# Kernel tuning notes

Measured on AMD Instinct MI355X. Metric: run time of the kernel, lower is better.

The kernel has to match this reference:

```python
import jax, jax.numpy as jnp
import numpy as np

ALPHA = 0.3
B, T, I, H = 256, 1024, 128, 1024


def setup_inputs() -> dict:
    key = jax.random.key(0)
    ks = jax.random.split(key, 7)
    s = 1.0 / np.sqrt(H)
    return {
        "x": jax.random.normal(ks[0], (B, T, I), dtype=jnp.float32),
        "W_ih": jax.random.normal(ks[1], (3 * H, I), dtype=jnp.float32) * s,
        "W_hh": jax.random.normal(ks[2], (3 * H, H), dtype=jnp.float32) * s,
        "b_ih": jax.random.normal(ks[3], (3 * H,), dtype=jnp.float32) * s,
        "b_hh": jax.random.normal(ks[4], (3 * H,), dtype=jnp.float32) * s,
        "W_fc": jax.random.normal(ks[5], (2, H), dtype=jnp.float32) * s,
        "b_fc": jax.random.normal(ks[6], (2,), dtype=jnp.float32) * s,
    }


def _forward(x, W_ih, W_hh, b_ih, b_hh, W_fc, b_fc):
    # --- ES normalize: s_i = (1-a)*x_i + a*s_{i-1}, s_0 = x_0 (in-place EMA) ---
    xs = jnp.swapaxes(x, 0, 1)  # [T, B, I]
    s0 = xs[0]

    def ema_step(s, xi):
        s2 = (1.0 - ALPHA) * xi + ALPHA * s
        return s2, s2

    _, rest = jax.lax.scan(ema_step, s0, xs[1:])
    sm = jnp.concatenate([s0[None], rest], axis=0)  # [T, B, I] smoothed
    st_1 = sm[-1]  # [B, I]

    # --- GRU (single layer, batch_first, h0 = 0); gate order r, z, n ---
    gi = jnp.einsum('tbi,gi->tbg', sm, W_ih) + b_ih  # [T, B, 3H]
    h0 = jnp.zeros((x.shape[0], W_hh.shape[1]), dtype=x.dtype)

    def gru_step(h, gi_t):
        gh = h @ W_hh.T + b_hh  # [B, 3H]
        i_r, i_z, i_n = jnp.split(gi_t, 3, axis=-1)
        h_r, h_z, h_n = jnp.split(gh, 3, axis=-1)
        r = jax.nn.sigmoid(i_r + h_r)
        z = jax.nn.sigmoid(i_z + h_z)
        n = jnp.tanh(i_n + r * h_n)
        h2 = (1.0 - z) * n + z * h
        return h2, None

    h_out, _ = jax.lax.scan(gru_step, h0, gi)  # [B, H]

    out = h_out @ W_fc.T + b_fc  # [B, 2]
    # --- ES denormalize with columns [1, 2] of st_1 ---
    out = (out - ALPHA * st_1[:, 1:3]) / (1.0 - ALPHA)
    return out


def reference(x, W_ih, W_hh, b_ih, b_hh, W_fc, b_fc):
    return _forward(x, W_ih, W_hh, b_ih, b_hh, W_fc, b_fc)
```

## Files before the change

kernel.cpp:

```cpp
#include <hip/hip_runtime.h>

typedef __attribute__((ext_vector_type(4))) float f4;
typedef __attribute__((ext_vector_type(8))) short frag8;
typedef unsigned long long u64;
typedef unsigned int u32;
typedef unsigned short u16;

#define ALPHA 0.3f

#define WHH_OFF   0ull
#define WIH_OFF   6291456ull
#define HBUF_OFF  7077888ull
#define CTR_OFF   8126464ull
#define ST1_OFF   8159232ull
#define ZERO_LEN  1083392ull

__device__ __forceinline__ u16 f2bf(float f) {
  u32 u = __float_as_uint(f);
  u32 r = (u + 0x7FFFu + ((u >> 16) & 1u)) >> 16;
  return (u16)r;
}
__device__ __forceinline__ float bf2f(u16 h) {
  return __uint_as_float(((u32)h) << 16);
}
__device__ __forceinline__ float sigmf(float x) {
  float e = __expf(-fabsf(x));
  float s = 1.0f / (1.0f + e);
  return x >= 0.f ? s : 1.0f - s;
}
__device__ __forceinline__ float tanhf_(float x) {
  float e = __expf(-2.0f * fabsf(x));
  float t = (1.0f - e) / (1.0f + e);
  return x >= 0.f ? t : -t;
}
__device__ __forceinline__ frag8 pack_bf16(f4 a, f4 b) {
  union { u16 h[8]; frag8 f; } u;
  u.h[0] = f2bf(a[0]); u.h[1] = f2bf(a[1]); u.h[2] = f2bf(a[2]); u.h[3] = f2bf(a[3]);
  u.h[4] = f2bf(b[0]); u.h[5] = f2bf(b[1]); u.h[6] = f2bf(b[2]); u.h[7] = f2bf(b[3]);
  return u.f;
}

__global__ void prep_bf16(const float* __restrict__ whh_f32,
                          const float* __restrict__ wih_f32,
                          u16* __restrict__ whh, u16* __restrict__ wih) {
  int i = blockIdx.x * 256 + threadIdx.x;
  const int nhh = 3072 * 1024;
  if (i < nhh) whh[i] = f2bf(whh_f32[i]);
  else         wih[i - nhh] = f2bf(wih_f32[i - nhh]);
}

__global__ __launch_bounds__(256, 1) void gru_kernel(
    const float* __restrict__ x,
    const float* __restrict__ b_ih,
    const float* __restrict__ b_hh,
    const u16* __restrict__ whh,
    const u16* __restrict__ wih,
    u64* __restrict__ hbuf,
    u32* __restrict__ ctr,
    float* __restrict__ st1)
{
  __shared__ f4 xbuf[4096];
  const int wg = blockIdx.x;
  const int g = wg >> 5, w = wg & 31;
  const int tid = threadIdx.x;
  const int v = tid >> 6;
  const int l = tid & 63;
  const int lm = l & 15, lq = l >> 4;

  frag8 whhf[8][6];
  frag8 wihf[6];
#pragma unroll
  for (int rt = 0; rt < 6; ++rt) {
    int grow = (rt >> 1) * 1024 + w * 32 + (rt & 1) * 16 + lm;
    wihf[rt] = *(const frag8*)(wih + grow * 128 + v * 32 + lq * 8);
#pragma unroll
    for (int kb = 0; kb < 8; ++kb)
      whhf[kb][rt] = *(const frag8*)(whh + grow * 1024 + v * 256 + kb * 32 + lq * 8);
  }

  const int uc = tid & 31;
  const int ub0 = (tid >> 5) << 2;
  const int colg = w * 32 + uc;
  const float bir = b_ih[colg],         bhr = b_hh[colg];
  const float biz = b_ih[1024 + colg],  bhz = b_hh[1024 + colg];
  const float bin_ = b_ih[2048 + colg], bhn = b_hh[2048 + colg];
  f4 hprev = {0.f, 0.f, 0.f, 0.f};

  f4 e0a, e0b, e1a, e1b;
  const float* xb0 = x + (size_t)(g * 32 + lm) * 131072 + v * 32 + lq * 8;
  const float* xb1 = x + (size_t)(g * 32 + 16 + lm) * 131072 + v * 32 + lq * 8;

  u32* cbase = ctr + g * 1024;
  const f4 zz = {0.f, 0.f, 0.f, 0.f};
  const float A1 = 1.0f - ALPHA;

#pragma unroll 1
  for (int t = 0; t < 1024; ++t) {
    u64* hread  = hbuf + (size_t)((t & 1) * 8 + g) * 8192;
    u64* hwrite = hbuf + (size_t)(((t + 1) & 1) * 8 + g) * 8192;

    frag8 af[8][2];
#pragma unroll
    for (int kb = 0; kb < 8; ++kb) {
#pragma unroll
      for (int bh = 0; bh < 2; ++bh) {
        int base = (((8 * v + kb) * 2 + bh) * 64 + l) * 2;
        union { u64 q[2]; frag8 f; } uu;
        uu.q[0] = __hip_atomic_load(hread + base,     __ATOMIC_RELAXED, __HIP_MEMORY_SCOPE_AGENT);
        uu.q[1] = __hip_atomic_load(hread + base + 1, __ATOMIC_RELAXED, __HIP_MEMORY_SCOPE_AGENT);
        af[kb][bh] = uu.f;
      }
    }

    {
      const float* xp0 = xb0 + (size_t)t * 128;
      const float* xp1 = xb1 + (size_t)t * 128;
      f4 xa0 = *(const f4*)xp0, xc0 = *(const f4*)(xp0 + 4);
      f4 xa1 = *(const f4*)xp1, xc1 = *(const f4*)(xp1 + 4);
      if (t == 0) { e0a = xa0; e0b = xc0; e1a = xa1; e1b = xc1; }
      else {
        e0a = A1 * xa0 + ALPHA * e0a; e0b = A1 * xc0 + ALPHA * e0b;
        e1a = A1 * xa1 + ALPHA * e1a; e1b = A1 * xc1 + ALPHA * e1b;
      }
    }
    if (t == 1023 && w == 0 && v == 0 && lq == 0) {
      st1[(g * 32 + lm) * 2 + 0] = e0a[1];
      st1[(g * 32 + lm) * 2 + 1] = e0a[2];
      st1[(g * 32 + 16 + lm) * 2 + 0] = e1a[1];
      st1[(g * 32 + 16 + lm) * 2 + 1] = e1a[2];
    }
    frag8 smf0 = pack_bf16(e0a, e0b);
    frag8 smf1 = pack_bf16(e1a, e1b);

    f4 acc[2][6], accn[2][2];
#pragma unroll
    for (int bh = 0; bh < 2; ++bh) {
#pragma unroll
      for (int rt = 0; rt < 6; ++rt) acc[bh][rt] = zz;
      accn[bh][0] = zz; accn[bh][1] = zz;
    }
#pragma unroll
    for (int rt = 0; rt < 4; ++rt) {
      acc[0][rt] = __builtin_amdgcn_mfma_f32_16x16x32_bf16(smf0, wihf[rt], acc[0][rt], 0, 0, 0);
      acc[1][rt] = __builtin_amdgcn_mfma_f32_16x16x32_bf16(smf1, wihf[rt], acc[1][rt], 0, 0, 0);
    }
#pragma unroll
    for (int nt = 0; nt < 2; ++nt) {
      accn[0][nt] = __builtin_amdgcn_mfma_f32_16x16x32_bf16(smf0, wihf[4 + nt], accn[0][nt], 0, 0, 0);
      accn[1][nt] = __builtin_amdgcn_mfma_f32_16x16x32_bf16(smf1, wihf[4 + nt], accn[1][nt], 0, 0, 0);
    }
#pragma unroll
    for (int kb = 0; kb < 8; ++kb) {
#pragma unroll
      for (int rt = 0; rt < 6; ++rt) {
        acc[0][rt] = __builtin_amdgcn_mfma_f32_16x16x32_bf16(af[kb][0], whhf[kb][rt], acc[0][rt], 0, 0, 0);
        acc[1][rt] = __builtin_amdgcn_mfma_f32_16x16x32_bf16(af[kb][1], whhf[kb][rt], acc[1][rt], 0, 0, 0);
      }
    }

#pragma unroll
    for (int bh = 0; bh < 2; ++bh) {
      int b8 = bh * 4 + lq;
#pragma unroll
      for (int rt = 0; rt < 6; ++rt) {
        int gr = rt * 16 + lm;
        xbuf[((v * 128 + gr) << 3) | (b8 ^ (gr & 7))] = acc[bh][rt];
      }
#pragma unroll
      for (int nt = 0; nt < 2; ++nt) {
        int gr = 96 + nt * 16 + lm;
        xbuf[((v * 128 + gr) << 3) | (b8 ^ (gr & 7))] = accn[bh][nt];
      }
    }
    __syncthreads();

    int swz = (ub0 >> 2) ^ (uc & 7);
    f4 sr = zz, sz4 = zz, gn4 = zz, gin4 = zz;
#pragma unroll
    for (int vv = 0; vv < 4; ++vv) {
      sr   += xbuf[((vv * 128 + uc) << 3) | swz];
      sz4  += xbuf[((vv * 128 + 32 + uc) << 3) | swz];
      gn4  += xbuf[((vv * 128 + 64 + uc) << 3) | swz];
      gin4 += xbuf[((vv * 128 + 96 + uc) << 3) | swz];
    }
    f4 h4;
#pragma unroll
    for (int i = 0; i < 4; ++i) {
      float rr = sigmf(sr[i] + bir + bhr);
      float zg = sigmf(sz4[i] + biz + bhz);
      float nn = tanhf_(gin4[i] + bin_ + rr * (gn4[i] + bhn));
      h4[i] = (1.0f - zg) * nn + zg * hprev[i];
    }
    hprev = h4;
    __syncthreads();

    u16* sbuf = (u16*)&xbuf[0];
#pragma unroll
    for (int i = 0; i < 4; ++i) sbuf[(ub0 + i) * 40 + uc] = f2bf(h4[i]);
    __syncthreads();
    {
      int b = tid >> 3, c0 = (tid & 7) << 2;
      u64 pk = *(const u64*)(sbuf + b * 40 + c0);
      int off = ((w * 2 + (b >> 4)) * 64 + (b & 15) + 16 * (c0 >> 3)) * 2 + ((c0 & 7) >> 2);
      __hip_atomic_store(hwrite + off, pk, __ATOMIC_RELAXED, __HIP_MEMORY_SCOPE_AGENT);
    }
    __syncthreads();

    if (tid == 0) {
      u32* cp = cbase + t;
      __hip_atomic_fetch_add(cp, 1u, __ATOMIC_RELEASE, __HIP_MEMORY_SCOPE_AGENT);
      while (__hip_atomic_load(cp, __ATOMIC_RELAXED, __HIP_MEMORY_SCOPE_AGENT) < 32u)
        __builtin_amdgcn_s_sleep(2);
      __builtin_amdgcn_fence(__ATOMIC_ACQUIRE, "agent");
    }
    __syncthreads();
  }
}

__global__ void fc_kernel(const u16* __restrict__ hbuf_bf,
                          const float* __restrict__ wfc,
                          const float* __restrict__ bfc,
                          const float* __restrict__ st1,
                          float* __restrict__ out)
{
  int b = blockIdx.x, t = threadIdx.x;
  int g = b >> 5, bl = b & 31, bh = bl >> 4;
  int k0 = t * 4, kb = k0 >> 5, ko = k0 & 31;
  int lane = (bl & 15) + 16 * (ko >> 3);
  const u16* hp = hbuf_bf + (size_t)g * 32768 + ((kb * 2 + bh) * 64 + lane) * 8 + (ko & 7);
  float h0 = bf2f(hp[0]), h1 = bf2f(hp[1]), h2 = bf2f(hp[2]), h3 = bf2f(hp[3]);
  float s0 = h0 * wfc[k0] + h1 * wfc[k0 + 1] + h2 * wfc[k0 + 2] + h3 * wfc[k0 + 3];
  float s1 = h0 * wfc[1024 + k0] + h1 * wfc[1024 + k0 + 1] +
             h2 * wfc[1024 + k0 + 2] + h3 * wfc[1024 + k0 + 3];
#pragma unroll
  for (int off = 32; off > 0; off >>= 1) {
    s0 += __shfl_down(s0, off);
    s1 += __shfl_down(s1, off);
  }
  __shared__ float red[8];
  if ((t & 63) == 0) { red[(t >> 6) * 2] = s0; red[(t >> 6) * 2 + 1] = s1; }
  __syncthreads();
  if (t == 0) {
    float a0 = red[0] + red[2] + red[4] + red[6] + bfc[0];
    float a1 = red[1] + red[3] + red[5] + red[7] + bfc[1];
    float inv = 1.0f / (1.0f - ALPHA);
    out[b * 2 + 0] = (a0 - ALPHA * st1[b * 2 + 0]) * inv;
    out[b * 2 + 1] = (a1 - ALPHA * st1[b * 2 + 1]) * inv;
  }
}

extern "C" void kernel_launch(void* const* d_in, const int* in_sizes, int n_in,
                              void* d_out, int out_size, void* d_ws, size_t ws_size,
                              hipStream_t stream) {
  const float* x   = (const float*)d_in[0];
  const float* Wih = (const float*)d_in[1];
  const float* Whh = (const float*)d_in[2];
  const float* bih = (const float*)d_in[3];
  const float* bhh = (const float*)d_in[4];
  const float* Wfc = (const float*)d_in[5];
  const float* bfc = (const float*)d_in[6];
  char* ws = (char*)d_ws;
  u16* whh_bf = (u16*)(ws + WHH_OFF);
  u16* wih_bf = (u16*)(ws + WIH_OFF);
  u64* hbuf   = (u64*)(ws + HBUF_OFF);
  u32* ctr    = (u32*)(ws + CTR_OFF);
  float* st1  = (float*)(ws + ST1_OFF);

  hipMemsetAsync(ws + HBUF_OFF, 0, ZERO_LEN, stream);
  prep_bf16<<<13824, 256, 0, stream>>>(Whh, Wih, whh_bf, wih_bf);
  gru_kernel<<<256, 256, 0, stream>>>(x, bih, bhh, whh_bf, wih_bf, hbuf, ctr, st1);
  fc_kernel<<<256, 256, 0, stream>>>((const u16*)(ws + HBUF_OFF), Wfc, bfc, st1,
                                     (float*)d_out);
}
```

Measured before the change: 9.300 ms.

## Replace atomic counter barrier with per-workgroup flags and overlap input projection

Measured after the change: 11.53 ms. +24.0%, slower.

```diff
diff --git a/kernel.cpp b/kernel.cpp
--- a/kernel.cpp
+++ b/kernel.cpp
@@ -11,9 +11,9 @@
 #define WHH_OFF   0ull
 #define WIH_OFF   6291456ull
 #define HBUF_OFF  7077888ull
-#define CTR_OFF   8126464ull
-#define ST1_OFF   8159232ull
-#define ZERO_LEN  1083392ull
+#define FLG_OFF   8126464ull
+#define ST1_OFF   8128512ull
+#define ZERO_LEN  1052672ull
 
 __device__ __forceinline__ u16 f2bf(float f) {
   u32 u = __float_as_uint(f);
@@ -56,10 +56,11 @@
     const u16* __restrict__ whh,
     const u16* __restrict__ wih,
     u64* __restrict__ hbuf,
-    u32* __restrict__ ctr,
+    u32* __restrict__ flags,
     float* __restrict__ st1)
 {
   __shared__ f4 xbuf[4096];
+  __shared__ u16 sbuf[32 * 40];
   const int wg = blockIdx.x;
   const int g = wg >> 5, w = wg & 31;
   const int tid = threadIdx.x;
@@ -90,9 +91,43 @@
   const float* xb0 = x + (size_t)(g * 32 + lm) * 131072 + v * 32 + lq * 8;
   const float* xb1 = x + (size_t)(g * 32 + 16 + lm) * 131072 + v * 32 + lq * 8;
 
-  u32* cbase = ctr + g * 1024;
+  u32* fbase = flags + g * 64;
   const f4 zz = {0.f, 0.f, 0.f, 0.f};
   const float A1 = 1.0f - ALPHA;
+
+  f4 acc[2][6], accn[2][2];
+
+  auto gi_compute = [&](int tt) {
+    const float* xp0 = xb0 + (size_t)tt * 128;
+    const float* xp1 = xb1 + (size_t)tt * 128;
+    f4 xa0 = *(const f4*)xp0, xc0 = *(const f4*)(xp0 + 4);
+    f4 xa1 = *(const f4*)xp1, xc1 = *(const f4*)(xp1 + 4);
+    if (tt == 0) { e0a = xa0; e0b = xc0; e1a = xa1; e1b = xc1; }
+    else {
+      e0a = A1 * xa0 + ALPHA * e0a; e0b = A1 * xc0 + ALPHA * e0b;
+      e1a = A1 * xa1 + ALPHA * e1a; e1b = A1 * xc1 + ALPHA * e1b;
+    }
+    frag8 smf0 = pack_bf16(e0a, e0b);
+    frag8 smf1 = pack_bf16(e1a, e1b);
+#pragma unroll
+    for (int bh = 0; bh < 2; ++bh) {
+#pragma unroll
+      for (int rt = 0; rt < 6; ++rt) acc[bh][rt] = zz;
+      accn[bh][0] = zz; accn[bh][1] = zz;
+    }
+#pragma unroll
+    for (int rt = 0; rt < 4; ++rt) {
+      acc[0][rt] = __builtin_amdgcn_mfma_f32_16x16x32_bf16(smf0, wihf[rt], acc[0][rt], 0, 0, 0);
+      acc[1][rt] = __builtin_amdgcn_mfma_f32_16x16x32_bf16(smf1, wihf[rt], acc[1][rt], 0, 0, 0);
+    }
+#pragma unroll
+    for (int nt = 0; nt < 2; ++nt) {
+      accn[0][nt] = __builtin_amdgcn_mfma_f32_16x16x32_bf16(smf0, wihf[4 + nt], accn[0][nt], 0, 0, 0);
+      accn[1][nt] = __builtin_amdgcn_mfma_f32_16x16x32_bf16(smf1, wihf[4 + nt], accn[1][nt], 0, 0, 0);
+    }
+  };
+
+  gi_compute(0);
 
 #pragma unroll 1
   for (int t = 0; t < 1024; ++t) {
@@ -111,44 +146,6 @@
         af[kb][bh] = uu.f;
       }
     }
-
-    {
-      const float* xp0 = xb0 + (size_t)t * 128;
-      const float* xp1 = xb1 + (size_t)t * 128;
-      f4 xa0 = *(const f4*)xp0, xc0 = *(const f4*)(xp0 + 4);
-      f4 xa1 = *(const f4*)xp1, xc1 = *(const f4*)(xp1 + 4);
-      if (t == 0) { e0a = xa0; e0b = xc0; e1a = xa1; e1b = xc1; }
-      else {
-        e0a = A1 * xa0 + ALPHA * e0a; e0b = A1 * xc0 + ALPHA * e0b;
-        e1a = A1 * xa1 + ALPHA * e1a; e1b = A1 * xc1 + ALPHA * e1b;
-      }
-    }
-    if (t == 1023 && w == 0 && v == 0 && lq == 0) {
-      st1[(g * 32 + lm) * 2 + 0] = e0a[1];
-      st1[(g * 32 + lm) * 2 + 1] = e0a[2];
-      st1[(g * 32 + 16 + lm) * 2 + 0] = e1a[1];
-      st1[(g * 32 + 16 + lm) * 2 + 1] = e1a[2];
-    }
-    frag8 smf0 = pack_bf16(e0a, e0b);
-    frag8 smf1 = pack_bf16(e1a, e1b);
-
-    f4 acc[2][6], accn[2][2];
-#pragma unroll
-    for (int bh = 0; bh < 2; ++bh) {
-#pragma unroll
-      for (int rt = 0; rt < 6; ++rt) acc[bh][rt] = zz;
-      accn[bh][0] = zz; accn[bh][1] = zz;
-    }
-#pragma unroll
-    for (int rt = 0; rt < 4; ++rt) {
-      acc[0][rt] = __builtin_amdgcn_mfma_f32_16x16x32_bf16(smf0, wihf[rt], acc[0][rt], 0, 0, 0);
-      acc[1][rt] = __builtin_amdgcn_mfma_f32_16x16x32_bf16(smf1, wihf[rt], acc[1][rt], 0, 0, 0);
-    }
-#pragma unroll
-    for (int nt = 0; nt < 2; ++nt) {
-      accn[0][nt] = __builtin_amdgcn_mfma_f32_16x16x32_bf16(smf0, wihf[4 + nt], accn[0][nt], 0, 0, 0);
-      accn[1][nt] = __builtin_amdgcn_mfma_f32_16x16x32_bf16(smf1, wihf[4 + nt], accn[1][nt], 0, 0, 0);
-    }
 #pragma unroll
     for (int kb = 0; kb < 8; ++kb) {
 #pragma unroll
@@ -192,9 +189,7 @@
       h4[i] = (1.0f - zg) * nn + zg * hprev[i];
     }
     hprev = h4;
-    __syncthreads();
-
-    u16* sbuf = (u16*)&xbuf[0];
+
 #pragma unroll
     for (int i = 0; i < 4; ++i) sbuf[(ub0 + i) * 40 + uc] = f2bf(h4[i]);
     __syncthreads();
@@ -206,14 +201,28 @@
     }
     __syncthreads();
 
-    if (tid == 0) {
-      u32* cp = cbase + t;
-      __hip_atomic_fetch_add(cp, 1u, __ATOMIC_RELEASE, __HIP_MEMORY_SCOPE_AGENT);
-      while (__hip_atomic_load(cp, __ATOMIC_RELAXED, __HIP_MEMORY_SCOPE_AGENT) < 32u)
-        __builtin_amdgcn_s_sleep(2);
+    if (tid == 0)
+      __hip_atomic_store(fbase + w, (u32)(t + 1), __ATOMIC_RELEASE, __HIP_MEMORY_SCOPE_AGENT);
+
+    if (t < 1023) gi_compute(t + 1);
+
+    if (v == 0) {
+      u32 tgt = (u32)(t + 1);
+      for (;;) {
+        u32 f = __hip_atomic_load(fbase + (l & 31), __ATOMIC_RELAXED, __HIP_MEMORY_SCOPE_AGENT);
+        if (__ballot(f < tgt) == 0) break;
+        __builtin_amdgcn_s_sleep(1);
+      }
       __builtin_amdgcn_fence(__ATOMIC_ACQUIRE, "agent");
     }
     __syncthreads();
+  }
+
+  if (w == 0 && v == 0 && lq == 0) {
+    st1[(g * 32 + lm) * 2 + 0] = e0a[1];
+    st1[(g * 32 + lm) * 2 + 1] = e0a[2];
+    st1[(g * 32 + 16 + lm) * 2 + 0] = e1a[1];
+    st1[(g * 32 + 16 + lm) * 2 + 1] = e1a[2];
   }
 }
 
@@ -263,12 +272,12 @@
   u16* whh_bf = (u16*)(ws + WHH_OFF);
   u16* wih_bf = (u16*)(ws + WIH_OFF);
   u64* hbuf   = (u64*)(ws + HBUF_OFF);
-  u32* ctr    = (u32*)(ws + CTR_OFF);
+  u32* flags  = (u32*)(ws + FLG_OFF);
   float* st1  = (float*)(ws + ST1_OFF);
 
   hipMemsetAsync(ws + HBUF_OFF, 0, ZERO_LEN, stream);
   prep_bf16<<<13824, 256, 0, stream>>>(Whh, Wih, whh_bf, wih_bf);
-  gru_kernel<<<256, 256, 0, stream>>>(x, bih, bhh, whh_bf, wih_bf, hbuf, ctr, st1);
+  gru_kernel<<<256, 256, 0, stream>>>(x, bih, bhh, whh_bf, wih_bf, hbuf, flags, st1);
   fc_kernel<<<256, 256, 0, stream>>>((const u16*)(ws + HBUF_OFF), Wfc, bfc, st1,
                                      (float*)d_out);
 }
```

## Replace per-step counter barrier with tagged h-state words and fine-grained polling

Applied to the files above, without the earlier changes.

Result: slower. 11.91 ms (+28.0%).

```diff
diff --git a/kernel.cpp b/kernel.cpp
--- a/kernel.cpp
+++ b/kernel.cpp
@@ -11,9 +11,8 @@
 #define WHH_OFF   0ull
 #define WIH_OFF   6291456ull
 #define HBUF_OFF  7077888ull
-#define CTR_OFF   8126464ull
-#define ST1_OFF   8159232ull
-#define ZERO_LEN  1083392ull
+#define ST1_OFF   9175040ull
+#define ZERO_LEN  2097152ull
 
 __device__ __forceinline__ u16 f2bf(float f) {
   u32 u = __float_as_uint(f);
@@ -56,10 +55,9 @@
     const u16* __restrict__ whh,
     const u16* __restrict__ wih,
     u64* __restrict__ hbuf,
-    u32* __restrict__ ctr,
     float* __restrict__ st1)
 {
-  __shared__ f4 xbuf[4096];
+  __shared__ f4 xbuf[8192];
   const int wg = blockIdx.x;
   const int g = wg >> 5, w = wg & 31;
   const int tid = threadIdx.x;
@@ -84,55 +82,51 @@
   const float bir = b_ih[colg],         bhr = b_hh[colg];
   const float biz = b_ih[1024 + colg],  bhz = b_hh[1024 + colg];
   const float bin_ = b_ih[2048 + colg], bhn = b_hh[2048 + colg];
+  const int cb = colg >> 5, lqw = (colg >> 3) & 3, jw = colg & 7;
   f4 hprev = {0.f, 0.f, 0.f, 0.f};
 
   f4 e0a, e0b, e1a, e1b;
   const float* xb0 = x + (size_t)(g * 32 + lm) * 131072 + v * 32 + lq * 8;
   const float* xb1 = x + (size_t)(g * 32 + 16 + lm) * 131072 + v * 32 + lq * 8;
-
-  u32* cbase = ctr + g * 1024;
+  f4 xn0 = *(const f4*)xb0, xn1 = *(const f4*)(xb0 + 4);
+  f4 xn2 = *(const f4*)xb1, xn3 = *(const f4*)(xb1 + 4);
+
+  const float A1 = 1.0f - ALPHA;
   const f4 zz = {0.f, 0.f, 0.f, 0.f};
-  const float A1 = 1.0f - ALPHA;
+  f4 acc[2][6], accn[2][2];
 
 #pragma unroll 1
   for (int t = 0; t < 1024; ++t) {
-    u64* hread  = hbuf + (size_t)((t & 1) * 8 + g) * 8192;
-    u64* hwrite = hbuf + (size_t)(((t + 1) & 1) * 8 + g) * 8192;
-
-    frag8 af[8][2];
-#pragma unroll
-    for (int kb = 0; kb < 8; ++kb) {
-#pragma unroll
-      for (int bh = 0; bh < 2; ++bh) {
-        int base = (((8 * v + kb) * 2 + bh) * 64 + l) * 2;
-        union { u64 q[2]; frag8 f; } uu;
-        uu.q[0] = __hip_atomic_load(hread + base,     __ATOMIC_RELAXED, __HIP_MEMORY_SCOPE_AGENT);
-        uu.q[1] = __hip_atomic_load(hread + base + 1, __ATOMIC_RELAXED, __HIP_MEMORY_SCOPE_AGENT);
-        af[kb][bh] = uu.f;
-      }
-    }
-
-    {
-      const float* xp0 = xb0 + (size_t)t * 128;
-      const float* xp1 = xb1 + (size_t)t * 128;
-      f4 xa0 = *(const f4*)xp0, xc0 = *(const f4*)(xp0 + 4);
-      f4 xa1 = *(const f4*)xp1, xc1 = *(const f4*)(xp1 + 4);
-      if (t == 0) { e0a = xa0; e0b = xc0; e1a = xa1; e1b = xc1; }
-      else {
-        e0a = A1 * xa0 + ALPHA * e0a; e0b = A1 * xc0 + ALPHA * e0b;
-        e1a = A1 * xa1 + ALPHA * e1a; e1b = A1 * xc1 + ALPHA * e1b;
-      }
-    }
-    if (t == 1023 && w == 0 && v == 0 && lq == 0) {
-      st1[(g * 32 + lm) * 2 + 0] = e0a[1];
-      st1[(g * 32 + lm) * 2 + 1] = e0a[2];
-      st1[(g * 32 + 16 + lm) * 2 + 0] = e1a[1];
-      st1[(g * 32 + 16 + lm) * 2 + 1] = e1a[2];
+    const u64* hread = hbuf + (size_t)((t & 1) * 8 + g) * 16384;
+    u32* hw32 = (u32*)(hbuf + (size_t)(((t + 1) & 1) * 8 + g) * 16384);
+    const u32 tg = (u32)t;
+    const u64 rep = (u64)tg | ((u64)tg << 32);
+
+    u64 q[4][8];
+#pragma unroll
+    for (int s = 0; s < 4; ++s) {
+      int base0 = (((v * 8 + s) * 2 + 0) * 16 + lm) * 16 + lq * 4;
+#pragma unroll
+      for (int j = 0; j < 4; ++j) {
+        q[s][j]     = __hip_atomic_load(hread + base0 + j,       __ATOMIC_RELAXED, __HIP_MEMORY_SCOPE_AGENT);
+        q[s][4 + j] = __hip_atomic_load(hread + base0 + 256 + j, __ATOMIC_RELAXED, __HIP_MEMORY_SCOPE_AGENT);
+      }
+    }
+
+    if (t == 0) { e0a = xn0; e0b = xn1; e1a = xn2; e1b = xn3; }
+    else {
+      e0a = A1 * xn0 + ALPHA * e0a; e0b = A1 * xn1 + ALPHA * e0b;
+      e1a = A1 * xn2 + ALPHA * e1a; e1b = A1 * xn3 + ALPHA * e1b;
     }
     frag8 smf0 = pack_bf16(e0a, e0b);
     frag8 smf1 = pack_bf16(e1a, e1b);
 
-    f4 acc[2][6], accn[2][2];
+    {
+      size_t to = (size_t)(t < 1023 ? t + 1 : 1023) * 128;
+      xn0 = *(const f4*)(xb0 + to); xn1 = *(const f4*)(xb0 + to + 4);
+      xn2 = *(const f4*)(xb1 + to); xn3 = *(const f4*)(xb1 + to + 4);
+    }
+
 #pragma unroll
     for (int bh = 0; bh < 2; ++bh) {
 #pragma unroll
@@ -149,27 +143,61 @@
       accn[0][nt] = __builtin_amdgcn_mfma_f32_16x16x32_bf16(smf0, wihf[4 + nt], accn[0][nt], 0, 0, 0);
       accn[1][nt] = __builtin_amdgcn_mfma_f32_16x16x32_bf16(smf1, wihf[4 + nt], accn[1][nt], 0, 0, 0);
     }
+
 #pragma unroll
     for (int kb = 0; kb < 8; ++kb) {
+      const int s = kb & 3;
+      for (;;) {
+        u64 bad = (q[s][0] ^ rep) | (q[s][1] ^ rep) | (q[s][2] ^ rep) | (q[s][3] ^ rep)
+                | (q[s][4] ^ rep) | (q[s][5] ^ rep) | (q[s][6] ^ rep) | (q[s][7] ^ rep);
+        bad &= 0x0000FFFF0000FFFFull;
+        if (__ballot(bad != 0ull) == 0ull) break;
+        int base0 = (((v * 8 + kb) * 2 + 0) * 16 + lm) * 16 + lq * 4;
+#pragma unroll
+        for (int j = 0; j < 4; ++j) {
+          q[s][j]     = __hip_atomic_load(hread + base0 + j,       __ATOMIC_RELAXED, __HIP_MEMORY_SCOPE_AGENT);
+          q[s][4 + j] = __hip_atomic_load(hread + base0 + 256 + j, __ATOMIC_RELAXED, __HIP_MEMORY_SCOPE_AGENT);
+        }
+      }
+      frag8 af0, af1;
+      {
+        union { u32 d[4]; frag8 f; } ua, ub;
+#pragma unroll
+        for (int j = 0; j < 4; ++j) {
+          ua.d[j] = __builtin_amdgcn_perm((u32)(q[s][j] >> 32),     (u32)q[s][j],     0x07060302u);
+          ub.d[j] = __builtin_amdgcn_perm((u32)(q[s][4 + j] >> 32), (u32)q[s][4 + j], 0x07060302u);
+        }
+        af0 = ua.f; af1 = ub.f;
+      }
+      if (kb < 4) {
+        int kn = kb + 4;
+        int base0 = (((v * 8 + kn) * 2 + 0) * 16 + lm) * 16 + lq * 4;
+#pragma unroll
+        for (int j = 0; j < 4; ++j) {
+          q[s][j]     = __hip_atomic_load(hread + base0 + j,       __ATOMIC_RELAXED, __HIP_MEMORY_SCOPE_AGENT);
+          q[s][4 + j] = __hip_atomic_load(hread + base0 + 256 + j, __ATOMIC_RELAXED, __HIP_MEMORY_SCOPE_AGENT);
+        }
+      }
 #pragma unroll
       for (int rt = 0; rt < 6; ++rt) {
-        acc[0][rt] = __builtin_amdgcn_mfma_f32_16x16x32_bf16(af[kb][0], whhf[kb][rt], acc[0][rt], 0, 0, 0);
-        acc[1][rt] = __builtin_amdgcn_mfma_f32_16x16x32_bf16(af[kb][1], whhf[kb][rt], acc[1][rt], 0, 0, 0);
-      }
-    }
-
+        acc[0][rt] = __builtin_amdgcn_mfma_f32_16x16x32_bf16(af0, whhf[kb][rt], acc[0][rt], 0, 0, 0);
+        acc[1][rt] = __builtin_amdgcn_mfma_f32_16x16x32_bf16(af1, whhf[kb][rt], acc[1][rt], 0, 0, 0);
+      }
+    }
+
+    f4* xb = xbuf + (t & 1) * 4096;
 #pragma unroll
     for (int bh = 0; bh < 2; ++bh) {
       int b8 = bh * 4 + lq;
 #pragma unroll
       for (int rt = 0; rt < 6; ++rt) {
         int gr = rt * 16 + lm;
-        xbuf[((v * 128 + gr) << 3) | (b8 ^ (gr & 7))] = acc[bh][rt];
+        xb[((v * 128 + gr) << 3) | (b8 ^ (gr & 7))] = acc[bh][rt];
       }
 #pragma unroll
       for (int nt = 0; nt < 2; ++nt) {
         int gr = 96 + nt * 16 + lm;
-        xbuf[((v * 128 + gr) << 3) | (b8 ^ (gr & 7))] = accn[bh][nt];
+        xb[((v * 128 + gr) << 3) | (b8 ^ (gr & 7))] = accn[bh][nt];
       }
     }
     __syncthreads();
@@ -178,10 +206,10 @@
     f4 sr = zz, sz4 = zz, gn4 = zz, gin4 = zz;
 #pragma unroll
     for (int vv = 0; vv < 4; ++vv) {
-      sr   += xbuf[((vv * 128 + uc) << 3) | swz];
-      sz4  += xbuf[((vv * 128 + 32 + uc) << 3) | swz];
-      gn4  += xbuf[((vv * 128 + 64 + uc) << 3) | swz];
-      gin4 += xbuf[((vv * 128 + 96 + uc) << 3) | swz];
+      sr   += xb[((vv * 128 + uc) << 3) | swz];
+      sz4  += xb[((vv * 128 + 32 + uc) << 3) | swz];
+      gn4  += xb[((vv * 128 + 64 + uc) << 3) | swz];
+      gin4 += xb[((vv * 128 + 96 + uc) << 3) | swz];
     }
     f4 h4;
 #pragma unroll
@@ -192,43 +220,38 @@
       h4[i] = (1.0f - zg) * nn + zg * hprev[i];
     }
     hprev = h4;
-    __syncthreads();
-
-    u16* sbuf = (u16*)&xbuf[0];
-#pragma unroll
-    for (int i = 0; i < 4; ++i) sbuf[(ub0 + i) * 40 + uc] = f2bf(h4[i]);
-    __syncthreads();
-    {
-      int b = tid >> 3, c0 = (tid & 7) << 2;
-      u64 pk = *(const u64*)(sbuf + b * 40 + c0);
-      int off = ((w * 2 + (b >> 4)) * 64 + (b & 15) + 16 * (c0 >> 3)) * 2 + ((c0 & 7) >> 2);
-      __hip_atomic_store(hwrite + off, pk, __ATOMIC_RELAXED, __HIP_MEMORY_SCOPE_AGENT);
-    }
-    __syncthreads();
-
-    if (tid == 0) {
-      u32* cp = cbase + t;
-      __hip_atomic_fetch_add(cp, 1u, __ATOMIC_RELEASE, __HIP_MEMORY_SCOPE_AGENT);
-      while (__hip_atomic_load(cp, __ATOMIC_RELAXED, __HIP_MEMORY_SCOPE_AGENT) < 32u)
-        __builtin_amdgcn_s_sleep(2);
-      __builtin_amdgcn_fence(__ATOMIC_ACQUIRE, "agent");
-    }
-    __syncthreads();
-  }
-}
-
-__global__ void fc_kernel(const u16* __restrict__ hbuf_bf,
+
+    u32 tgw = (u32)(t + 1) & 0xFFFFu;
+#pragma unroll
+    for (int i = 0; i < 4; ++i) {
+      int b = ub0 + i;
+      u32 val = ((u32)f2bf(h4[i]) << 16) | tgw;
+      int idx = ((cb * 2 + (b >> 4)) * 16 + (b & 15)) * 32 + lqw * 8 + jw;
+      __hip_atomic_store(hw32 + idx, val, __ATOMIC_RELAXED, __HIP_MEMORY_SCOPE_AGENT);
+    }
+  }
+
+  if (w == 0 && v == 0 && lq == 0) {
+    st1[(g * 32 + lm) * 2 + 0] = e0a[1];
+    st1[(g * 32 + lm) * 2 + 1] = e0a[2];
+    st1[(g * 32 + 16 + lm) * 2 + 0] = e1a[1];
+    st1[(g * 32 + 16 + lm) * 2 + 1] = e1a[2];
+  }
+}
+
+__global__ void fc_kernel(const u32* __restrict__ hbuf32,
                           const float* __restrict__ wfc,
                           const float* __restrict__ bfc,
                           const float* __restrict__ st1,
                           float* __restrict__ out)
 {
   int b = blockIdx.x, t = threadIdx.x;
-  int g = b >> 5, bl = b & 31, bh = bl >> 4;
-  int k0 = t * 4, kb = k0 >> 5, ko = k0 & 31;
-  int lane = (bl & 15) + 16 * (ko >> 3);
-  const u16* hp = hbuf_bf + (size_t)g * 32768 + ((kb * 2 + bh) * 64 + lane) * 8 + (ko & 7);
-  float h0 = bf2f(hp[0]), h1 = bf2f(hp[1]), h2 = bf2f(hp[2]), h3 = bf2f(hp[3]);
+  int g = b >> 5, bl = b & 31;
+  int k0 = t * 4;
+  int idx = (((k0 >> 5) * 2 + (bl >> 4)) * 16 + (bl & 15)) * 32 + ((k0 >> 3) & 3) * 8 + (k0 & 7);
+  const u32* hp = hbuf32 + (size_t)g * 32768 + idx;
+  float h0 = bf2f((u16)(hp[0] >> 16)), h1 = bf2f((u16)(hp[1] >> 16));
+  float h2 = bf2f((u16)(hp[2] >> 16)), h3 = bf2f((u16)(hp[3] >> 16));
   float s0 = h0 * wfc[k0] + h1 * wfc[k0 + 1] + h2 * wfc[k0 + 2] + h3 * wfc[k0 + 3];
   float s1 = h0 * wfc[1024 + k0] + h1 * wfc[1024 + k0 + 1] +
              h2 * wfc[1024 + k0 + 2] + h3 * wfc[1024 + k0 + 3];
@@ -263,12 +286,11 @@
   u16* whh_bf = (u16*)(ws + WHH_OFF);
   u16* wih_bf = (u16*)(ws + WIH_OFF);
   u64* hbuf   = (u64*)(ws + HBUF_OFF);
-  u32* ctr    = (u32*)(ws + CTR_OFF);
   float* st1  = (float*)(ws + ST1_OFF);
 
   hipMemsetAsync(ws + HBUF_OFF, 0, ZERO_LEN, stream);
   prep_bf16<<<13824, 256, 0, stream>>>(Whh, Wih, whh_bf, wih_bf);
-  gru_kernel<<<256, 256, 0, stream>>>(x, bih, bhh, whh_bf, wih_bf, hbuf, ctr, st1);
-  fc_kernel<<<256, 256, 0, stream>>>((const u16*)(ws + HBUF_OFF), Wfc, bfc, st1,
+  gru_kernel<<<256, 256, 0, stream>>>(x, bih, bhh, whh_bf, wih_bf, hbuf, st1);
+  fc_kernel<<<256, 256, 0, stream>>>((const u32*)(ws + HBUF_OFF), Wfc, bfc, st1,
                                      (float*)d_out);
 }
```
